# Performance work log

Hardware: AMD Instinct MI355X
Metric: run time of the kernel (lower is better)

## Reference

```python
import jax, jax.numpy as jnp
import numpy as np

ATOM = 8          # atom_size
STRIDE = 4
NB_ATOMS = 256
LMBDA = 0.1       # l1 prox weight (prox_params)
NONDIFF = 20      # nondiff_steps (run under stop_gradient, mirroring torch.no_grad)
DIFF = 5          # diff_steps


def setup_inputs() -> dict:
    key = jax.random.key(0)
    k1, k2 = jax.random.split(key)
    y = jax.random.normal(k1, (8, 3, 256, 256), dtype=jnp.float32)
    # atoms ~ N(0,1)/sqrt(nb_channels*atom_size^2), as in __init__ with init='random'
    atoms = jax.random.normal(k2, (NB_ATOMS, 3, ATOM, ATOM), dtype=jnp.float32) / np.float32(np.sqrt(3 * ATOM * ATOM))
    return {"y": y, "atoms": atoms}


def _forward(y, atoms):
    B, C, H, W = y.shape
    a, s = ATOM, STRIDE
    Hp = (H - a) // s + 1
    Wp = (W - a) // s + 1
    D = C * a * a

    # patch row/col index grids: rows[ph, i] = ph*s + i
    rows = (jnp.arange(Hp) * s)[:, None] + jnp.arange(a)          # [Hp, a]
    cols = (jnp.arange(Wp) * s)[:, None] + jnp.arange(a)          # [Wp, a]
    R4 = rows[:, :, None, None]                                    # [Hp, a, 1, 1]
    C4 = cols[None, None, :, :]                                    # [1, 1, Wp, a]

    # unfold: extract overlapping patches -> [B, C, Hp, a, Wp, a] -> [N, D] (channel-major, matching torch)
    p6 = y[:, :, R4, C4]
    p = p6.transpose(0, 2, 4, 1, 3, 5).reshape(B * Hp * Wp, D)     # N = B*Hp*Wp

    mean = jnp.mean(p, axis=1, keepdims=True)                      # per-patch mean
    p = p - mean

    # l2-normalize atoms
    A = atoms.reshape(NB_ATOMS, D)
    A = A / jnp.linalg.norm(A, axis=1, keepdims=True)              # [nA, D]

    X = A @ A.T                                                    # [nA, nA] Gram matrix
    q = A @ p.T                                                    # [nA, N]
    L = jnp.linalg.norm(X, 2)                                      # spectral norm (Lipschitz const)
    thr = LMBDA / L

    def ista_step(c, _):
        c = c - (X @ c - q) / L
        c = jnp.sign(c) * jnp.maximum(jnp.abs(c) - thr, 0.0)       # soft-threshold prox
        return c, None

    c0 = jnp.zeros((NB_ATOMS, q.shape[1]), dtype=q.dtype)
    c, _ = jax.lax.scan(ista_step, c0, None, length=NONDIFF)
    c = jax.lax.stop_gradient(c)                                    # torch.no_grad() warmup
    c, _ = jax.lax.scan(ista_step, c, None, length=DIFF)

    # reconstruct patches: einsum('ij,il->jl') = c.T @ A, add mean back
    rec = c.T @ A + mean                                            # [N, D]
    p6r = rec.reshape(B, Hp, Wp, C, a, a).transpose(0, 3, 1, 4, 2, 5)  # [B, C, Hp, a, Wp, a]

    # fold: overlap-add patches back to image
    out = jnp.zeros((B, C, H, W), dtype=y.dtype).at[:, :, R4, C4].add(p6r)
    counts = jnp.zeros((H, W), dtype=y.dtype).at[R4, C4].add(
        jnp.ones((Hp, a, Wp, a), dtype=y.dtype))                    # overlap divisors
    return out / counts


def reference(y, atoms):
    return _forward(y, atoms)
```

## Files before the change

### kernel.cpp

```cpp
#include <hip/hip_runtime.h>
#include <math.h>

#define NPATCH 31752
#define TILE   64
#define PSTR   200
#define MSTR   200

typedef _Float16 f16;
typedef __attribute__((ext_vector_type(2))) _Float16 f16x2;
typedef __attribute__((ext_vector_type(4))) _Float16 f16x4;
typedef __attribute__((ext_vector_type(8))) _Float16 f16x8;
typedef __attribute__((ext_vector_type(2))) __fp16   hf16x2;
typedef __attribute__((ext_vector_type(4))) float    f32x4;
#define MFMA16 __builtin_amdgcn_mfma_f32_16x16x32_f16

union HU { f16x2 h; hf16x2 g; unsigned u; };

__device__ __forceinline__ f16x2 pk2(float a, float b)
{
    HU r; r.g = __builtin_amdgcn_cvt_pkrtz(a, b);
    return r.h;
}

__device__ __forceinline__ f16x2 shrink2(f16x2 v, f16x2 thr2)
{
    HU a; a.h = v;
    unsigned sgn = a.u & 0x80008000u;
    a.u &= 0x7FFF7FFFu;
    f16x2 t = a.h - thr2;
    t = __builtin_elementwise_max(t, (f16x2)(f16)0);
    HU r; r.h = t; r.u |= sgn;
    return r.h;
}

__global__ void fusedpack_kernel(const float* __restrict__ atoms,
                                 float* __restrict__ A, float* __restrict__ As,
                                 f16* __restrict__ Ap, f16* __restrict__ Ab)
{
    __shared__ float part[6];
    const int b = blockIdx.x, t = threadIdx.x;
    float v = atoms[b*192 + t];
    float s = v*v, r = v;
    #pragma unroll
    for (int m = 1; m < 64; m <<= 1) { s += __shfl_xor(s, m, 64); r += __shfl_xor(r, m, 64); }
    const int wv = t >> 6, lane = t & 63;
    if (lane == 0) { part[wv] = s; part[3 + wv] = r; }
    __syncthreads();
    s = part[0] + part[1] + part[2];
    r = part[3] + part[4] + part[5];
    float rn = 1.0f / sqrtf(s);
    float a  = v * rn;
    A[b*192 + t] = a;
    if (t == 0) As[b] = r * rn;
    f16 ah = (f16)a;
    {
        int I = b >> 4, l16 = b & 15;
        int ks = t >> 5, q = (t >> 3) & 3, j = t & 7;
        Ap[(((I*6 + ks)*64) + q*16 + l16)*8 + j] = ah;
    }
    {
        int dt = t >> 4, dl = t & 15;
        int ks = b >> 5, q = (b >> 3) & 3, j = b & 7;
        Ab[(((dt*8 + ks)*64) + q*16 + dl)*8 + j] = ah;
    }
}

__global__ __launch_bounds__(512, 1)
void lchain_kernel(const f16* __restrict__ Ab, float* __restrict__ scal)
{
    __shared__ f16   mls[2 * 192 * MSTR];
    __shared__ float red[8];
    __shared__ float trc[16];
    const int tid = threadIdx.x, wv = tid >> 6, lane = tid & 63;
    const int quad = lane >> 4, l16 = lane & 15;
    const int g3 = (wv >> 1) * 3;
    const int h6 = (wv & 1) * 6;
    const f16x8* AbV = (const f16x8*)Ab;

    f32x4 acc[3][6];
    #pragma unroll
    for (int it = 0; it < 3; ++it)
        #pragma unroll
        for (int jj = 0; jj < 6; ++jj) acc[it][jj] = (f32x4){0,0,0,0};
    for (int ks = 0; ks < 8; ++ks) {
        f16x8 bf[6];
        #pragma unroll
        for (int jj = 0; jj < 6; ++jj) bf[jj] = AbV[((h6 + jj)*8 + ks)*64 + lane];
        #pragma unroll
        for (int it = 0; it < 3; ++it) {
            f16x8 af = AbV[((g3 + it)*8 + ks)*64 + lane];
            #pragma unroll
            for (int jj = 0; jj < 6; ++jj)
                acc[it][jj] = MFMA16(af, bf[jj], acc[it][jj], 0, 0, 0);
        }
    }
    #pragma unroll
    for (int it = 0; it < 3; ++it) {
        int I = g3 + it;
        #pragma unroll
        for (int jj = 0; jj < 6; ++jj) {
            int J = h6 + jj;
            f16x2 lo = pk2(acc[it][jj][0], acc[it][jj][1]);
            f16x2 hi = pk2(acc[it][jj][2], acc[it][jj][3]);
            f16x4 cc; cc[0]=lo[0]; cc[1]=lo[1]; cc[2]=hi[0]; cc[3]=hi[1];
            *(f16x4*)&mls[(J*16 + l16)*MSTR + I*16 + quad*4] = cc;
        }
    }
    __syncthreads();

    float rprev = 1.0f;
    for (int t = 1; t <= 8; ++t) {
        const f16* src = mls + ((t & 1) ^ 1) * (192 * MSTR);
        f16*       dst = mls + (t & 1) * (192 * MSTR);
        const float inv = 1.0f / rprev;
        const float inv2 = inv * inv;

        f32x4 a2[3][6];
        #pragma unroll
        for (int it = 0; it < 3; ++it)
            #pragma unroll
            for (int jj = 0; jj < 6; ++jj) a2[it][jj] = (f32x4){0,0,0,0};
        for (int ksd = 0; ksd < 6; ++ksd) {
            f16x8 bf[6];
            #pragma unroll
            for (int jj = 0; jj < 6; ++jj)
                bf[jj] = *(const f16x8*)&src[((h6 + jj)*16 + l16)*MSTR + ksd*32 + quad*8];
            #pragma unroll
            for (int it = 0; it < 3; ++it) {
                f16x8 af = *(const f16x8*)&src[((g3 + it)*16 + l16)*MSTR + ksd*32 + quad*8];
                #pragma unroll
                for (int jj = 0; jj < 6; ++jj)
                    a2[it][jj] = MFMA16(af, bf[jj], a2[it][jj], 0, 0, 0);
            }
        }
        float dsum = 0.0f;
        #pragma unroll
        for (int it = 0; it < 3; ++it) {
            int I = g3 + it;
            #pragma unroll
            for (int jj = 0; jj < 6; ++jj) {
                int J = h6 + jj;
                float v0 = a2[it][jj][0] * inv2;
                float v1 = a2[it][jj][1] * inv2;
                float v2 = a2[it][jj][2] * inv2;
                float v3 = a2[it][jj][3] * inv2;
                f16x2 lo = pk2(v0, v1);
                f16x2 hi = pk2(v2, v3);
                f16x4 cc; cc[0]=lo[0]; cc[1]=lo[1]; cc[2]=hi[0]; cc[3]=hi[1];
                *(f16x4*)&dst[(J*16 + l16)*MSTR + I*16 + quad*4] = cc;
                if (J == I) {
                    int dg = l16 - quad*4;
                    if (dg >= 0 && dg < 4)
                        dsum += (dg == 0 ? v0 : dg == 1 ? v1 : dg == 2 ? v2 : v3);
                }
            }
        }
        #pragma unroll
        for (int m = 1; m < 64; m <<= 1) dsum += __shfl_xor(dsum, m, 64);
        if (lane == 0) red[wv] = dsum;
        __syncthreads();
        float r = red[0] + red[1] + red[2] + red[3]
                + red[4] + red[5] + red[6] + red[7];
        if (tid == 0) trc[t] = r;
        rprev = r;
        __syncthreads();
    }
    if (tid == 0) {
        float a = 0.0f;
        #pragma unroll
        for (int u = 1; u <= 8; ++u) a += exp2f(-(float)u) * log2f(trc[u]);
        float L = exp2f(a);
        scal[16] = 1.0f / L;
        scal[17] = 0.1f / L;
    }
}

__global__ void gpack_kernel(const float* __restrict__ A, const float* __restrict__ scal,
                             f16* __restrict__ Gp)
{
    __shared__ float arow[192];
    __shared__ float xrow[256];
    int i = blockIdx.x, j = threadIdx.x;
    const float invL = scal[16];
    if (j < 192) arow[j] = A[i*192 + j];
    __syncthreads();
    float s = 0.0f;
    #pragma unroll 4
    for (int d = 0; d < 192; d += 4) {
        float4 av = *(const float4*)&A[j*192 + d];
        s += arow[d]*av.x + arow[d+1]*av.y + arow[d+2]*av.z + arow[d+3]*av.w;
    }
    xrow[j] = (i == j ? 1.0f : 0.0f) - s * invL;
    __syncthreads();
    if (j < 32) {
        int ks = j >> 2, q = j & 3;
        f16x8 h;
        #pragma unroll
        for (int u = 0; u < 8; ++u) h[u] = (f16)xrow[ks*32 + q*8 + u];
        int I = i >> 4, lane = q*16 + (i & 15);
        *(f16x8*)&Gp[(((I*8 + ks)*64) + lane)*8] = h;
    }
}

__global__ __launch_bounds__(256, 2)
void mega_kernel(const float* __restrict__ y,
                 const f16* __restrict__ Gp, const f16* __restrict__ Ap,
                 const f16* __restrict__ Ab, const float* __restrict__ As,
                 const float* __restrict__ scal, float* __restrict__ out)
{
    __shared__ f16      p_lds[TILE * PSTR];
    __shared__ f16      c_lds[2 * 16 * 512];
    __shared__ float    mean_lds[TILE];
    __shared__ float    msum[512];
    __shared__ unsigned pco[TILE];

    const int tid  = threadIdx.x;
    const int base = blockIdx.x * TILE;
    const int wv = tid >> 6, lane = tid & 63, quad = lane >> 4, l16 = lane & 15;
    const float invL = scal[16];
    const float thr  = scal[17];
    const f16x2 thr2 = { (f16)thr, (f16)thr };

    #define CWADDR(st, rt, ct) \
        ((st)*8192 + ((ct)*8 + (wv*2 + ((rt)>>1)))*512 \
         + ((((rt)&1)*2 + (quad>>1))*16 + l16)*8 + (quad&1)*4)

    f16x8 greg[4][8];
    {
        const f16x8* GpV = (const f16x8*)Gp;
        #pragma unroll
        for (int rt = 0; rt < 4; ++rt)
            #pragma unroll
            for (int ks = 0; ks < 8; ++ks)
                greg[rt][ks] = GpV[((wv*4 + rt)*8 + ks)*64 + lane];
    }

    #pragma unroll
    for (int p = 0; p < 2; ++p) {
        int n_l = p*32 + (tid >> 3), qq = tid & 7;
        int n = base + n_l; if (n >= NPATCH) n = NPATCH - 1;
        int b = n / 3969, rem = n - b * 3969;
        int r = rem / 63, sc = rem - r * 63;
        if (qq == 0) pco[n_l] = ((unsigned)b << 16) | ((unsigned)r << 8) | (unsigned)sc;
        float s = 0.0f;
        #pragma unroll
        for (int u = 0; u < 3; ++u) {
            int d  = qq * 24 + u * 8;
            int ch = d >> 6, id = (d & 63) >> 3;
            const float* src = &y[((b*3 + ch)*256 + (r*4 + id))*256 + sc*4];
            float4 a = *(const float4*)src;
            float4 bq = *(const float4*)(src + 4);
            s += a.x + a.y + a.z + a.w + bq.x + bq.y + bq.z + bq.w;
            f16x8 h = { (f16)a.x, (f16)a.y, (f16)a.z, (f16)a.w,
                        (f16)bq.x, (f16)bq.y, (f16)bq.z, (f16)bq.w };
            *(f16x8*)&p_lds[n_l * PSTR + d] = h;
        }
        msum[p*256 + tid] = s;
    }
    __syncthreads();
    if (tid < TILE) {
        int p = tid >> 5, bse = (tid & 31) * 8;
        float s = 0.0f;
        #pragma unroll
        for (int u = 0; u < 8; ++u) s += msum[p*256 + bse + u];
        mean_lds[tid] = s * (1.0f / 192.0f);
    }
    __syncthreads();

    f16x2 qslo[2][4][2], qshi[2][4][2];
    const f16x8* ApV = (const f16x8*)Ap;
    #pragma unroll
    for (int st = 0; st < 2; ++st) {
        f32x4 qf[4][2];
        #pragma unroll
        for (int rt = 0; rt < 4; ++rt)
            #pragma unroll
            for (int ct = 0; ct < 2; ++ct) qf[rt][ct] = (f32x4){0,0,0,0};
        #pragma unroll
        for (int ks = 0; ks < 6; ++ks) {
            f16x8 bf[2];
            #pragma unroll
            for (int ct = 0; ct < 2; ++ct)
                bf[ct] = *(const f16x8*)&p_lds[(st*32 + ct*16 + l16)*PSTR + ks*32 + quad*8];
            #pragma unroll
            for (int rt = 0; rt < 4; ++rt) {
                f16x8 af = ApV[((wv*4 + rt)*6 + ks)*64 + lane];
                #pragma unroll
                for (int ct = 0; ct < 2; ++ct)
                    qf[rt][ct] = MFMA16(af, bf[ct], qf[rt][ct], 0, 0, 0);
            }
        }
        #pragma unroll
        for (int rt = 0; rt < 4; ++rt) {
            float a0 = As[wv*64 + rt*16 + quad*4 + 0];
            float a1 = As[wv*64 + rt*16 + quad*4 + 1];
            float a2 = As[wv*64 + rt*16 + quad*4 + 2];
            float a3 = As[wv*64 + rt*16 + quad*4 + 3];
            #pragma unroll
            for (int ct = 0; ct < 2; ++ct) {
                float mn = mean_lds[st*32 + ct*16 + l16];
                float q0 = (qf[rt][ct][0] - mn*a0) * invL;
                float q1 = (qf[rt][ct][1] - mn*a1) * invL;
                float q2 = (qf[rt][ct][2] - mn*a2) * invL;
                float q3 = (qf[rt][ct][3] - mn*a3) * invL;
                f16x2 lo = pk2(q0, q1);
                f16x2 hi = pk2(q2, q3);
                qslo[st][rt][ct] = lo;  qshi[st][rt][ct] = hi;
                f16x2 clo = shrink2(lo, thr2);
                f16x2 chi = shrink2(hi, thr2);
                f16x4 cc; cc[0]=clo[0]; cc[1]=clo[1]; cc[2]=chi[0]; cc[3]=chi[1];
                *(f16x4*)&c_lds[CWADDR(st, rt, ct)] = cc;
            }
        }
    }
    __syncthreads();

    for (int it = 0; it < 24; ++it) {
        f32x4 af[4][2];
        #pragma unroll
        for (int rt = 0; rt < 4; ++rt)
            #pragma unroll
            for (int ct = 0; ct < 2; ++ct) af[rt][ct] = (f32x4){0,0,0,0};
        #pragma unroll
        for (int ks = 0; ks < 8; ++ks) {
            f16x8 b0 = *(const f16x8*)&c_lds[(ks)*512 + lane*8];
            f16x8 b1 = *(const f16x8*)&c_lds[(8 + ks)*512 + lane*8];
            #pragma unroll
            for (int rt = 0; rt < 4; ++rt) {
                af[rt][0] = MFMA16(greg[rt][ks], b0, af[rt][0], 0, 0, 0);
                af[rt][1] = MFMA16(greg[rt][ks], b1, af[rt][1], 0, 0, 0);
            }
        }
        __syncthreads();
        #pragma unroll
        for (int rt = 0; rt < 4; ++rt)
            #pragma unroll
            for (int ct = 0; ct < 2; ++ct) {
                f16x2 vlo = pk2(af[rt][ct][0], af[rt][ct][1]) + qslo[0][rt][ct];
                f16x2 vhi = pk2(af[rt][ct][2], af[rt][ct][3]) + qshi[0][rt][ct];
                vlo = shrink2(vlo, thr2);
                vhi = shrink2(vhi, thr2);
                f16x4 cc; cc[0]=vlo[0]; cc[1]=vlo[1]; cc[2]=vhi[0]; cc[3]=vhi[1];
                *(f16x4*)&c_lds[CWADDR(0, rt, ct)] = cc;
            }
        #pragma unroll
        for (int rt = 0; rt < 4; ++rt)
            #pragma unroll
            for (int ct = 0; ct < 2; ++ct) af[rt][ct] = (f32x4){0,0,0,0};
        #pragma unroll
        for (int ks = 0; ks < 8; ++ks) {
            f16x8 b0 = *(const f16x8*)&c_lds[8192 + (ks)*512 + lane*8];
            f16x8 b1 = *(const f16x8*)&c_lds[8192 + (8 + ks)*512 + lane*8];
            #pragma unroll
            for (int rt = 0; rt < 4; ++rt) {
                af[rt][0] = MFMA16(greg[rt][ks], b0, af[rt][0], 0, 0, 0);
                af[rt][1] = MFMA16(greg[rt][ks], b1, af[rt][1], 0, 0, 0);
            }
        }
        __syncthreads();
        #pragma unroll
        for (int rt = 0; rt < 4; ++rt)
            #pragma unroll
            for (int ct = 0; ct < 2; ++ct) {
                f16x2 vlo = pk2(af[rt][ct][0], af[rt][ct][1]) + qslo[1][rt][ct];
                f16x2 vhi = pk2(af[rt][ct][2], af[rt][ct][3]) + qshi[1][rt][ct];
                vlo = shrink2(vlo, thr2);
                vhi = shrink2(vhi, thr2);
                f16x4 cc; cc[0]=vlo[0]; cc[1]=vlo[1]; cc[2]=vhi[0]; cc[3]=vhi[1];
                *(f16x4*)&c_lds[CWADDR(1, rt, ct)] = cc;
            }
    }
    __syncthreads();

    const int nt = wv >> 1, dtb = 6 * (wv & 1);
    const f16x8* AbV = (const f16x8*)Ab;
    #pragma unroll
    for (int st = 0; st < 2; ++st) {
        f32x4 rf[6];
        #pragma unroll
        for (int u = 0; u < 6; ++u) rf[u] = (f32x4){0,0,0,0};
        #pragma unroll
        for (int ks = 0; ks < 8; ++ks) {
            f16x8 afr = *(const f16x8*)&c_lds[st*8192 + (nt*8 + ks)*512 + lane*8];
            #pragma unroll
            for (int u = 0; u < 6; ++u) {
                f16x8 bb = AbV[((dtb + u)*8 + ks)*64 + lane];
                rf[u] = MFMA16(afr, bb, rf[u], 0, 0, 0);
            }
        }
        #pragma unroll
        for (int g = 0; g < 4; ++g) {
            int nl = nt*16 + quad*4 + g;
            int n  = base + st*32 + nl;
            if (n < NPATCH) {
                unsigned pc = pco[st*32 + nl];
                int b = pc >> 16, r = (pc >> 8) & 255, sc = pc & 255;
                float mn = mean_lds[st*32 + nl];
                #pragma unroll
                for (int u = 0; u < 6; ++u) {
                    int d  = (dtb + u)*16 + l16;
                    int ch = d >> 6, dh = (d & 63) >> 3, dw = d & 7;
                    int h  = r*4 + dh, w2 = sc*4 + dw;
                    int cnth = min(62, h >> 2)  - (max(h - 4, 0) >> 2) + 1;
                    int cntw = min(62, w2 >> 2) - (max(w2 - 4, 0) >> 2) + 1;
                    float rcp = 1.0f / (float)(cnth * cntw);
                    atomicAdd(&out[((b*3 + ch)*256 + (r*4 + dh))*256 + sc*4 + dw],
                              (rf[u][g] + mn) * rcp);
                }
            }
        }
    }
    #undef CWADDR
}

extern "C" void kernel_launch(void* const* d_in, const int* in_sizes, int n_in,
                              void* d_out, int out_size, void* d_ws, size_t ws_size,
                              hipStream_t stream)
{
    const float* y     = (const float*)d_in[0];
    const float* atoms = (const float*)d_in[1];
    float* out = (float*)d_out;
    float* ws  = (float*)d_ws;

    float* A    = ws;
    float* As   = ws + 49152;
    float* scal = ws + 49408;
    f16*   Ap   = (f16*)(ws + 49440);
    f16*   Ab   = (f16*)(ws + 74016);
    f16*   Gp   = (f16*)(ws + 98592);

    (void)hipMemsetAsync(d_out, 0, (size_t)out_size * sizeof(float), stream);

    fusedpack_kernel<<<256, 192, 0, stream>>>(atoms, A, As, Ap, Ab);
    lchain_kernel   <<<1, 512,   0, stream>>>(Ab, scal);
    gpack_kernel    <<<256, 256, 0, stream>>>(A, scal, Gp);
    mega_kernel     <<<(NPATCH + TILE - 1) / TILE, 256, 0, stream>>>
        (y, Gp, Ap, Ab, As, scal, out);
}
```

Measured before the change: 205.1 us.

## Fuse atom prep into lchain, fold memset into gpack, widen mega kernel to 512 threads

Atom normalization and packing move into the single-block lchain kernel, and output zeroing moves into gpack, which removes one launch and the memset. The mega kernel now runs 512 threads per block, so each wave owns half as many Gram-row tiles and the register footprint shrinks, which allows more waves per CU. It also computes the patch mean with shuffles instead of an LDS reduction, loads As as a float4, and raises wave priority around the MFMA loops. The risks are that atom prep becomes serial inside a single block, and the wider blocks carry more barrier cost per iteration.

```diff
diff --git a/kernel.cpp b/kernel.cpp
--- a/kernel.cpp
+++ b/kernel.cpp
@@ -33,46 +33,47 @@
     return r.h;
 }
 
-__global__ void fusedpack_kernel(const float* __restrict__ atoms,
-                                 float* __restrict__ A, float* __restrict__ As,
-                                 f16* __restrict__ Ap, f16* __restrict__ Ab)
-{
-    __shared__ float part[6];
-    const int b = blockIdx.x, t = threadIdx.x;
-    float v = atoms[b*192 + t];
-    float s = v*v, r = v;
-    #pragma unroll
-    for (int m = 1; m < 64; m <<= 1) { s += __shfl_xor(s, m, 64); r += __shfl_xor(r, m, 64); }
-    const int wv = t >> 6, lane = t & 63;
-    if (lane == 0) { part[wv] = s; part[3 + wv] = r; }
-    __syncthreads();
-    s = part[0] + part[1] + part[2];
-    r = part[3] + part[4] + part[5];
-    float rn = 1.0f / sqrtf(s);
-    float a  = v * rn;
-    A[b*192 + t] = a;
-    if (t == 0) As[b] = r * rn;
-    f16 ah = (f16)a;
-    {
-        int I = b >> 4, l16 = b & 15;
-        int ks = t >> 5, q = (t >> 3) & 3, j = t & 7;
-        Ap[(((I*6 + ks)*64) + q*16 + l16)*8 + j] = ah;
-    }
-    {
-        int dt = t >> 4, dl = t & 15;
-        int ks = b >> 5, q = (b >> 3) & 3, j = b & 7;
-        Ab[(((dt*8 + ks)*64) + q*16 + dl)*8 + j] = ah;
-    }
-}
-
 __global__ __launch_bounds__(512, 1)
-void lchain_kernel(const f16* __restrict__ Ab, float* __restrict__ scal)
+void lchain_kernel(const float* __restrict__ atoms,
+                   float* __restrict__ A, float* __restrict__ As,
+                   f16* __restrict__ Ap, f16* __restrict__ Ab,
+                   float* __restrict__ scal)
 {
     __shared__ f16   mls[2 * 192 * MSTR];
     __shared__ float red[8];
     __shared__ float trc[16];
     const int tid = threadIdx.x, wv = tid >> 6, lane = tid & 63;
     const int quad = lane >> 4, l16 = lane & 15;
+
+    for (int rr = 0; rr < 32; ++rr) {
+        int b = wv*32 + rr;
+        float v0 = atoms[b*192 + lane];
+        float v1 = atoms[b*192 +  64 + lane];
+        float v2 = atoms[b*192 + 128 + lane];
+        float s = v0*v0 + v1*v1 + v2*v2;
+        float r = v0 + v1 + v2;
+        #pragma unroll
+        for (int m = 1; m < 64; m <<= 1) { s += __shfl_xor(s, m, 64); r += __shfl_xor(r, m, 64); }
+        float rn = 1.0f / sqrtf(s);
+        if (lane == 0) As[b] = r * rn;
+        const int I = b >> 4, l16b = b & 15;
+        const int ksb = b >> 5, qb = (b >> 3) & 3, jb = b & 7;
+        float vv[3] = { v0, v1, v2 };
+        #pragma unroll
+        for (int u = 0; u < 3; ++u) {
+            int t = u*64 + lane;
+            float a = vv[u] * rn;
+            A[b*192 + t] = a;
+            f16 ah = (f16)a;
+            int ks = t >> 5, q = (t >> 3) & 3, j = t & 7;
+            Ap[((I*6 + ks)*64 + q*16 + l16b)*8 + j] = ah;
+            int dt = t >> 4, dl = t & 15;
+            Ab[((dt*8 + ksb)*64 + qb*16 + dl)*8 + jb] = ah;
+        }
+    }
+    __threadfence_block();
+    __syncthreads();
+
     const int g3 = (wv >> 1) * 3;
     const int h6 = (wv & 1) * 6;
     const f16x8* AbV = (const f16x8*)Ab;
@@ -176,10 +177,19 @@
 }
 
 __global__ void gpack_kernel(const float* __restrict__ A, const float* __restrict__ scal,
-                             f16* __restrict__ Gp)
+                             f16* __restrict__ Gp, float* __restrict__ out, int out_n)
 {
     __shared__ float arow[192];
     __shared__ float xrow[256];
+    {
+        float4* o4 = (float4*)out;
+        int idx = blockIdx.x * blockDim.x + threadIdx.x;
+        int tot4 = out_n >> 2;
+        for (int u = idx; u < tot4; u += gridDim.x * blockDim.x)
+            o4[u] = (float4){0.f, 0.f, 0.f, 0.f};
+        for (int u = (tot4 << 2) + idx; u < out_n; u += gridDim.x * blockDim.x)
+            out[u] = 0.f;
+    }
     int i = blockIdx.x, j = threadIdx.x;
     const float invL = scal[16];
     if (j < 192) arow[j] = A[i*192 + j];
@@ -202,7 +212,7 @@
     }
 }
 
-__global__ __launch_bounds__(256, 2)
+__global__ __launch_bounds__(512, 4)
 void mega_kernel(const float* __restrict__ y,
                  const f16* __restrict__ Gp, const f16* __restrict__ Ap,
                  const f16* __restrict__ Ab, const float* __restrict__ As,
@@ -211,7 +221,6 @@
     __shared__ f16      p_lds[TILE * PSTR];
     __shared__ f16      c_lds[2 * 16 * 512];
     __shared__ float    mean_lds[TILE];
-    __shared__ float    msum[512];
     __shared__ unsigned pco[TILE];
 
     const int tid  = threadIdx.x;
@@ -222,26 +231,24 @@
     const f16x2 thr2 = { (f16)thr, (f16)thr };
 
     #define CWADDR(st, rt, ct) \
-        ((st)*8192 + ((ct)*8 + (wv*2 + ((rt)>>1)))*512 \
-         + ((((rt)&1)*2 + (quad>>1))*16 + l16)*8 + (quad&1)*4)
-
-    f16x8 greg[4][8];
+        ((st)*8192 + ((ct)*8 + wv)*512 \
+         + (((rt)*2 + (quad>>1))*16 + l16)*8 + (quad&1)*4)
+
+    f16x8 greg[2][8];
     {
         const f16x8* GpV = (const f16x8*)Gp;
         #pragma unroll
-        for (int rt = 0; rt < 4; ++rt)
+        for (int rt = 0; rt < 2; ++rt)
             #pragma unroll
             for (int ks = 0; ks < 8; ++ks)
-                greg[rt][ks] = GpV[((wv*4 + rt)*8 + ks)*64 + lane];
-    }
-
-    #pragma unroll
-    for (int p = 0; p < 2; ++p) {
-        int n_l = p*32 + (tid >> 3), qq = tid & 7;
+                greg[rt][ks] = GpV[((wv*2 + rt)*8 + ks)*64 + lane];
+    }
+
+    {
+        int n_l = tid >> 3, qq = tid & 7;
         int n = base + n_l; if (n >= NPATCH) n = NPATCH - 1;
         int b = n / 3969, rem = n - b * 3969;
         int r = rem / 63, sc = rem - r * 63;
-        if (qq == 0) pco[n_l] = ((unsigned)b << 16) | ((unsigned)r << 8) | (unsigned)sc;
         float s = 0.0f;
         #pragma unroll
         for (int u = 0; u < 3; ++u) {
@@ -255,25 +262,23 @@
                         (f16)bq.x, (f16)bq.y, (f16)bq.z, (f16)bq.w };
             *(f16x8*)&p_lds[n_l * PSTR + d] = h;
         }
-        msum[p*256 + tid] = s;
-    }
-    __syncthreads();
-    if (tid < TILE) {
-        int p = tid >> 5, bse = (tid & 31) * 8;
-        float s = 0.0f;
-        #pragma unroll
-        for (int u = 0; u < 8; ++u) s += msum[p*256 + bse + u];
-        mean_lds[tid] = s * (1.0f / 192.0f);
-    }
-    __syncthreads();
-
-    f16x2 qslo[2][4][2], qshi[2][4][2];
+        s += __shfl_xor(s, 1, 64);
+        s += __shfl_xor(s, 2, 64);
+        s += __shfl_xor(s, 4, 64);
+        if (qq == 0) {
+            mean_lds[n_l] = s * (1.0f / 192.0f);
+            pco[n_l] = ((unsigned)b << 16) | ((unsigned)r << 8) | (unsigned)sc;
+        }
+    }
+    __syncthreads();
+
+    f16x2 qslo[2][2][2], qshi[2][2][2];
     const f16x8* ApV = (const f16x8*)Ap;
     #pragma unroll
     for (int st = 0; st < 2; ++st) {
-        f32x4 qf[4][2];
-        #pragma unroll
-        for (int rt = 0; rt < 4; ++rt)
+        f32x4 qf[2][2];
+        #pragma unroll
+        for (int rt = 0; rt < 2; ++rt)
             #pragma unroll
             for (int ct = 0; ct < 2; ++ct) qf[rt][ct] = (f32x4){0,0,0,0};
         #pragma unroll
@@ -283,26 +288,23 @@
             for (int ct = 0; ct < 2; ++ct)
                 bf[ct] = *(const f16x8*)&p_lds[(st*32 + ct*16 + l16)*PSTR + ks*32 + quad*8];
             #pragma unroll
-            for (int rt = 0; rt < 4; ++rt) {
-                f16x8 af = ApV[((wv*4 + rt)*6 + ks)*64 + lane];
+            for (int rt = 0; rt < 2; ++rt) {
+                f16x8 af = ApV[((wv*2 + rt)*6 + ks)*64 + lane];
                 #pragma unroll
                 for (int ct = 0; ct < 2; ++ct)
                     qf[rt][ct] = MFMA16(af, bf[ct], qf[rt][ct], 0, 0, 0);
             }
         }
         #pragma unroll
-        for (int rt = 0; rt < 4; ++rt) {
-            float a0 = As[wv*64 + rt*16 + quad*4 + 0];
-            float a1 = As[wv*64 + rt*16 + quad*4 + 1];
-            float a2 = As[wv*64 + rt*16 + quad*4 + 2];
-            float a3 = As[wv*64 + rt*16 + quad*4 + 3];
+        for (int rt = 0; rt < 2; ++rt) {
+            float4 av = *(const float4*)&As[(wv*2 + rt)*16 + quad*4];
             #pragma unroll
             for (int ct = 0; ct < 2; ++ct) {
                 float mn = mean_lds[st*32 + ct*16 + l16];
-                float q0 = (qf[rt][ct][0] - mn*a0) * invL;
-                float q1 = (qf[rt][ct][1] - mn*a1) * invL;
-                float q2 = (qf[rt][ct][2] - mn*a2) * invL;
-                float q3 = (qf[rt][ct][3] - mn*a3) * invL;
+                float q0 = (qf[rt][ct][0] - mn*av.x) * invL;
+                float q1 = (qf[rt][ct][1] - mn*av.y) * invL;
+                float q2 = (qf[rt][ct][2] - mn*av.z) * invL;
+                float q3 = (qf[rt][ct][3] - mn*av.w) * invL;
                 f16x2 lo = pk2(q0, q1);
                 f16x2 hi = pk2(q2, q3);
                 qslo[st][rt][ct] = lo;  qshi[st][rt][ct] = hi;
@@ -316,24 +318,26 @@
     __syncthreads();
 
     for (int it = 0; it < 24; ++it) {
-        f32x4 af[4][2];
-        #pragma unroll
-        for (int rt = 0; rt < 4; ++rt)
+        f32x4 af[2][2];
+        #pragma unroll
+        for (int rt = 0; rt < 2; ++rt)
             #pragma unroll
             for (int ct = 0; ct < 2; ++ct) af[rt][ct] = (f32x4){0,0,0,0};
+        __builtin_amdgcn_s_setprio(1);
         #pragma unroll
         for (int ks = 0; ks < 8; ++ks) {
             f16x8 b0 = *(const f16x8*)&c_lds[(ks)*512 + lane*8];
             f16x8 b1 = *(const f16x8*)&c_lds[(8 + ks)*512 + lane*8];
             #pragma unroll
-            for (int rt = 0; rt < 4; ++rt) {
+            for (int rt = 0; rt < 2; ++rt) {
                 af[rt][0] = MFMA16(greg[rt][ks], b0, af[rt][0], 0, 0, 0);
                 af[rt][1] = MFMA16(greg[rt][ks], b1, af[rt][1], 0, 0, 0);
             }
         }
+        __builtin_amdgcn_s_setprio(0);
         __syncthreads();
         #pragma unroll
-        for (int rt = 0; rt < 4; ++rt)
+        for (int rt = 0; rt < 2; ++rt)
             #pragma unroll
             for (int ct = 0; ct < 2; ++ct) {
                 f16x2 vlo = pk2(af[rt][ct][0], af[rt][ct][1]) + qslo[0][rt][ct];
@@ -344,22 +348,24 @@
                 *(f16x4*)&c_lds[CWADDR(0, rt, ct)] = cc;
             }
         #pragma unroll
-        for (int rt = 0; rt < 4; ++rt)
+        for (int rt = 0; rt < 2; ++rt)
             #pragma unroll
             for (int ct = 0; ct < 2; ++ct) af[rt][ct] = (f32x4){0,0,0,0};
+        __builtin_amdgcn_s_setprio(1);
         #pragma unroll
         for (int ks = 0; ks < 8; ++ks) {
             f16x8 b0 = *(const f16x8*)&c_lds[8192 + (ks)*512 + lane*8];
             f16x8 b1 = *(const f16x8*)&c_lds[8192 + (8 + ks)*512 + lane*8];
             #pragma unroll
-            for (int rt = 0; rt < 4; ++rt) {
+            for (int rt = 0; rt < 2; ++rt) {
                 af[rt][0] = MFMA16(greg[rt][ks], b0, af[rt][0], 0, 0, 0);
                 af[rt][1] = MFMA16(greg[rt][ks], b1, af[rt][1], 0, 0, 0);
             }
         }
+        __builtin_amdgcn_s_setprio(0);
         __syncthreads();
         #pragma unroll
-        for (int rt = 0; rt < 4; ++rt)
+        for (int rt = 0; rt < 2; ++rt)
             #pragma unroll
             for (int ct = 0; ct < 2; ++ct) {
                 f16x2 vlo = pk2(af[rt][ct][0], af[rt][ct][1]) + qslo[1][rt][ct];
@@ -372,18 +378,18 @@
     }
     __syncthreads();
 
-    const int nt = wv >> 1, dtb = 6 * (wv & 1);
+    const int nt = wv >> 2, dtb = 3 * (wv & 3);
     const f16x8* AbV = (const f16x8*)Ab;
     #pragma unroll
     for (int st = 0; st < 2; ++st) {
-        f32x4 rf[6];
-        #pragma unroll
-        for (int u = 0; u < 6; ++u) rf[u] = (f32x4){0,0,0,0};
+        f32x4 rf[3];
+        #pragma unroll
+        for (int u = 0; u < 3; ++u) rf[u] = (f32x4){0,0,0,0};
         #pragma unroll
         for (int ks = 0; ks < 8; ++ks) {
             f16x8 afr = *(const f16x8*)&c_lds[st*8192 + (nt*8 + ks)*512 + lane*8];
             #pragma unroll
-            for (int u = 0; u < 6; ++u) {
+            for (int u = 0; u < 3; ++u) {
                 f16x8 bb = AbV[((dtb + u)*8 + ks)*64 + lane];
                 rf[u] = MFMA16(afr, bb, rf[u], 0, 0, 0);
             }
@@ -397,7 +403,7 @@
                 int b = pc >> 16, r = (pc >> 8) & 255, sc = pc & 255;
                 float mn = mean_lds[st*32 + nl];
                 #pragma unroll
-                for (int u = 0; u < 6; ++u) {
+                for (int u = 0; u < 3; ++u) {
                     int d  = (dtb + u)*16 + l16;
                     int ch = d >> 6, dh = (d & 63) >> 3, dw = d & 7;
                     int h  = r*4 + dh, w2 = sc*4 + dw;
@@ -429,11 +435,8 @@
     f16*   Ab   = (f16*)(ws + 74016);
     f16*   Gp   = (f16*)(ws + 98592);
 
-    (void)hipMemsetAsync(d_out, 0, (size_t)out_size * sizeof(float), stream);
-
-    fusedpack_kernel<<<256, 192, 0, stream>>>(atoms, A, As, Ap, Ab);
-    lchain_kernel   <<<1, 512,   0, stream>>>(Ab, scal);
-    gpack_kernel    <<<256, 256, 0, stream>>>(A, scal, Gp);
-    mega_kernel     <<<(NPATCH + TILE - 1) / TILE, 256, 0, stream>>>
+    lchain_kernel<<<1, 512, 0, stream>>>(atoms, A, As, Ap, Ab, scal);
+    gpack_kernel <<<256, 256, 0, stream>>>(A, scal, Gp, out, out_size);
+    mega_kernel  <<<(NPATCH + TILE - 1) / TILE, 512, 0, stream>>>
         (y, Gp, Ap, Ab, As, scal, out);
 }
```

New measurement: 222.7 us. 1.09x slower.
